# Kernel optimization log

Measured on AMD Instinct MI355X. Metric: run time of the kernel, lower is better.

Reference implementation:

```python
import jax, jax.numpy as jnp
import numpy as np

D_MODEL = 1024
N_HEADS = 16
HEAD_DIM = D_MODEL // N_HEADS
FFN_DIM = 4096
T = 2048
LN_EPS = 1e-5


def layer_norm(x, g, b):
    mu = jnp.mean(x, axis=-1, keepdims=True)
    var = jnp.mean(jnp.square(x - mu), axis=-1, keepdims=True)
    return (x - mu) * jax.lax.rsqrt(var + LN_EPS) * g + b


def setup_inputs() -> dict:
    key = jax.random.key(0)
    ks = jax.random.split(key, 12)
    s = 0.02
    x = jax.random.normal(ks[0], (1, T, D_MODEL), dtype=jnp.float32)
    # causal mask: True means masked (strict upper triangle)
    causal_mask = jnp.triu(jnp.ones((T, T), dtype=bool), k=1)
    # ALiBi bias: -slope * distance, per head
    slopes = 2.0 ** (-8.0 * (jnp.arange(1, N_HEADS + 1, dtype=jnp.float32) / N_HEADS))
    pos = jnp.arange(T, dtype=jnp.float32)
    dist = pos[None, :] - pos[:, None]  # (T, T)
    alibi_bias = slopes[:, None, None] * jnp.minimum(dist, 0.0)[None]  # (H, T, T)
    inp = {
        "x": x,
        "causal_mask": causal_mask,
        "alibi_bias": alibi_bias.astype(jnp.float32),
        "wq": jax.random.normal(ks[1], (D_MODEL, D_MODEL), jnp.float32) * s,
        "bq": jnp.zeros((D_MODEL,), jnp.float32),
        "wk": jax.random.normal(ks[2], (D_MODEL, D_MODEL), jnp.float32) * s,
        "bk": jnp.zeros((D_MODEL,), jnp.float32),
        "wv": jax.random.normal(ks[3], (D_MODEL, D_MODEL), jnp.float32) * s,
        "bv": jnp.zeros((D_MODEL,), jnp.float32),
        "wo": jax.random.normal(ks[4], (D_MODEL, D_MODEL), jnp.float32) * s,
        "bo": jnp.zeros((D_MODEL,), jnp.float32),
        "w1": jax.random.normal(ks[5], (D_MODEL, FFN_DIM), jnp.float32) * s,
        "b1": jnp.zeros((FFN_DIM,), jnp.float32),
        "w2": jax.random.normal(ks[6], (FFN_DIM, D_MODEL), jnp.float32) * s,
        "b2": jnp.zeros((D_MODEL,), jnp.float32),
        "g1": jnp.ones((D_MODEL,), jnp.float32),
        "be1": jnp.zeros((D_MODEL,), jnp.float32),
        "g2": jnp.ones((D_MODEL,), jnp.float32),
        "be2": jnp.zeros((D_MODEL,), jnp.float32),
    }
    return inp


def reference(x, causal_mask, alibi_bias, wq, bq, wk, bk, wv, bv, wo, bo,
              w1, b1, w2, b2, g1, be1, g2, be2):
    B, Tt, D = x.shape
    H, hd = N_HEADS, HEAD_DIM
    x_norm = layer_norm(x, g1, be1)
    # projections -> (B, H, T, hd)
    def split_heads(y):
        return y.reshape(B, Tt, H, hd).transpose(0, 2, 1, 3)
    Q = split_heads(x_norm @ wq + bq)
    K = split_heads(x_norm @ wk + bk)
    V = split_heads(x_norm @ wv + bv)
    scale = jnp.sqrt(jnp.float32(hd))
    scores = jnp.einsum('bhqd,bhkd->bhqk', Q, K) / scale
    scores = scores + alibi_bias[None]
    scores = jnp.where(causal_mask[None, None], -jnp.inf, scores)
    attn = jax.nn.softmax(scores, axis=-1)
    attn_out = jnp.einsum('bhqk,bhkd->bhqd', attn, V)
    attn_out = attn_out.transpose(0, 2, 1, 3).reshape(B, Tt, D)
    attn_out = attn_out @ wo + bo
    x = x + attn_out
    x_norm = layer_norm(x, g2, be2)
    h = jax.nn.gelu(x_norm @ w1 + b1, approximate=False)
    ffn_out = h @ w2 + b2
    return x + ffn_out
```

## Files before the change

### kernel.cpp

```cpp
#include <hip/hip_runtime.h>
#include <hip/hip_bf16.h>
#include <math.h>

#define T_SEQ 2048
#define D_MODEL 1024
#define N_HEADS 16
#define HEAD_DIM 64
#define FFN_DIM 4096

typedef _Float16 halfx8 __attribute__((ext_vector_type(8)));
typedef _Float16 halfx4 __attribute__((ext_vector_type(4)));
typedef float floatx4 __attribute__((ext_vector_type(4)));

__device__ __forceinline__ void async_ld16(const _Float16* g, _Float16* l) {
  __builtin_amdgcn_global_load_lds(
      (const __attribute__((address_space(1))) unsigned int*)g,
      (__attribute__((address_space(3))) unsigned int*)l, 16, 0, 0);
}

__global__ __launch_bounds__(256) void ln_h_kernel(
    const float* __restrict__ x, const float* __restrict__ g,
    const float* __restrict__ b, _Float16* __restrict__ y, int D) {
  int row = blockIdx.x;
  const float* xr = x + (size_t)row * D;
  _Float16* yr = y + (size_t)row * D;
  int tid = threadIdx.x;
  int lid = tid & 63, wid = tid >> 6;
  __shared__ float red[8];

  float sum = 0.f;
  for (int i = tid; i < D; i += 256) sum += xr[i];
  for (int o = 32; o > 0; o >>= 1) sum += __shfl_down(sum, o, 64);
  if (lid == 0) red[wid] = sum;
  __syncthreads();
  if (tid == 0) { float t = 0; for (int i = 0; i < 4; i++) t += red[i]; red[0] = t; }
  __syncthreads();
  float mu = red[0] / D;
  __syncthreads();

  float vs = 0.f;
  for (int i = tid; i < D; i += 256) { float d = xr[i] - mu; vs += d * d; }
  for (int o = 32; o > 0; o >>= 1) vs += __shfl_down(vs, o, 64);
  if (lid == 0) red[wid] = vs;
  __syncthreads();
  if (tid == 0) { float t = 0; for (int i = 0; i < 4; i++) t += red[i]; red[0] = t; }
  __syncthreads();
  float rstd = rsqrtf(red[0] / D + 1e-5f);

  for (int i = tid; i < D; i += 256)
    yr[i] = (_Float16)((xr[i] - mu) * rstd * g[i] + b[i]);
}

__global__ __launch_bounds__(256) void transpose_h_kernel(
    const float* __restrict__ in, _Float16* __restrict__ out, int K, int N) {
  __shared__ float tile[32][33];
  int tk = blockIdx.y * 32, tn = blockIdx.x * 32;
  int tid = threadIdx.x;
  int r = tid >> 3;
  int c = (tid & 7) * 4;
  float4 v = *(const float4*)&in[(size_t)(tk + r) * N + tn + c];
  tile[r][c] = v.x; tile[r][c + 1] = v.y; tile[r][c + 2] = v.z; tile[r][c + 3] = v.w;
  __syncthreads();
  halfx4 o;
  o[0] = (_Float16)tile[c][r];
  o[1] = (_Float16)tile[c + 1][r];
  o[2] = (_Float16)tile[c + 2][r];
  o[3] = (_Float16)tile[c + 3][r];
  *(halfx4*)&out[(size_t)(tn + r) * K + tk + c] = o;
}

__global__ __launch_bounds__(256) void pack_bias_kernel(
    const float* __restrict__ bq, const float* __restrict__ bk,
    const float* __restrict__ bv, float* __restrict__ o) {
  int i = blockIdx.x * 256 + threadIdx.x;
  if (i < 1024) o[i] = bq[i];
  else if (i < 2048) o[i] = bk[i - 1024];
  else if (i < 3072) o[i] = bv[i - 2048];
}

template <int MODE>
__global__ __launch_bounds__(256) void hgemm_kernel(
    const _Float16* __restrict__ A, const _Float16* __restrict__ Bt,
    const float* __restrict__ bias, const float* __restrict__ res,
    float* __restrict__ Cf, _Float16* __restrict__ Ch,
    int M, int N, int K) {
  __shared__ _Float16 As[128][32];
  __shared__ _Float16 Bs[128][32];
  const int tid = threadIdx.x;
  const int w = tid >> 6, lane = tid & 63;
  const int l16 = lane & 15, quad = lane >> 4;
  const int m0 = blockIdx.y * 128, n0 = blockIdx.x * 128;
  const int wm = (w >> 1) * 64, wn = (w & 1) * 64;

  floatx4 acc[4][4];
#pragma unroll
  for (int i = 0; i < 4; i++)
#pragma unroll
    for (int j = 0; j < 4; j++) acc[i][j] = (floatx4){0.f, 0.f, 0.f, 0.f};

  const int srow = lane >> 2;
  const int scol = (lane & 3) * 8;
  const _Float16* Ag = A + (size_t)(m0 + w * 32 + srow) * K + scol;
  const _Float16* Bg = Bt + (size_t)(n0 + w * 32 + srow) * K + scol;
  _Float16* AsB = &As[w * 32][0];
  _Float16* BsB = &Bs[w * 32][0];

  for (int k0 = 0; k0 < K; k0 += 32) {
    async_ld16(Ag + k0, AsB);
    async_ld16(Ag + k0 + (size_t)16 * K, AsB + 16 * 32);
    async_ld16(Bg + k0, BsB);
    async_ld16(Bg + k0 + (size_t)16 * K, BsB + 16 * 32);
    __syncthreads();
    halfx8 af[4], bf[4];
#pragma unroll
    for (int mt = 0; mt < 4; mt++) af[mt] = *(const halfx8*)&As[wm + mt * 16 + l16][quad * 8];
#pragma unroll
    for (int nt = 0; nt < 4; nt++) bf[nt] = *(const halfx8*)&Bs[wn + nt * 16 + l16][quad * 8];
#pragma unroll
    for (int mt = 0; mt < 4; mt++)
#pragma unroll
      for (int nt = 0; nt < 4; nt++)
        acc[mt][nt] = __builtin_amdgcn_mfma_f32_16x16x32_f16(af[mt], bf[nt], acc[mt][nt], 0, 0, 0);
    __syncthreads();
  }

#pragma unroll
  for (int mt = 0; mt < 4; mt++) {
#pragma unroll
    for (int nt = 0; nt < 4; nt++) {
      int col = n0 + wn + nt * 16 + l16;
      float bv = bias[col];
#pragma unroll
      for (int r = 0; r < 4; r++) {
        int row = m0 + wm + mt * 16 + quad * 4 + r;
        float v = acc[mt][nt][r] + bv;
        if (MODE == 1) v = 0.5f * v * (1.0f + erff(v * 0.70710678118f));
        if (MODE == 2) {
          Cf[(size_t)row * N + col] = v + res[(size_t)row * N + col];
        } else {
          Ch[(size_t)row * N + col] = (_Float16)v;
        }
      }
    }
  }
}

#define LROW 72
#define QKV_STR 3072
__global__ __launch_bounds__(256) void flash_attn_kernel(
    const _Float16* __restrict__ QKV, _Float16* __restrict__ out) {
  __shared__ _Float16 Ks[64][LROW];
  __shared__ _Float16 Vt[64][LROW];
  __shared__ _Float16 Ps[4][16][LROW];

  const int h = blockIdx.y;
  const int qt = blockIdx.x;
  const int q0 = qt * 64;
  const int tid = threadIdx.x;
  const int w = tid >> 6;
  const int lane = tid & 63;
  const int l16 = lane & 15;
  const int quad = lane >> 4;

  const _Float16* Qg = QKV + h * HEAD_DIM;
  const _Float16* Kg = QKV + 1024 + h * HEAD_DIM;
  const _Float16* Vg = QKV + 2048 + h * HEAD_DIM;

  const _Float16* qp = Qg + (size_t)(q0 + w * 16 + l16) * QKV_STR;
  halfx8 qa0 = *(const halfx8*)(qp + quad * 8);
  halfx8 qa1 = *(const halfx8*)(qp + 32 + quad * 8);

  float m_i[4], l_i[4];
  floatx4 o_acc[4];
#pragma unroll
  for (int r = 0; r < 4; r++) { m_i[r] = -INFINITY; l_i[r] = 0.f; }
#pragma unroll
  for (int c = 0; c < 4; c++) o_acc[c] = (floatx4){0.f, 0.f, 0.f, 0.f};

  const float slope = exp2f(-0.5f * (float)(h + 1));
  const int row_base = q0 + w * 16 + quad * 4;

  for (int t = 0; t <= qt; t++) {
    const int k0 = t * 64;
    __syncthreads();
#pragma unroll
    for (int it = 0; it < 2; it++) {
      int chunk = tid + it * 256;
      int kr = chunk >> 3, c8 = chunk & 7;
      *(halfx8*)(&Ks[kr][c8 * 8]) =
          *(const halfx8*)(Kg + (size_t)(k0 + kr) * QKV_STR + c8 * 8);
    }
#pragma unroll
    for (int it = 0; it < 2; it++) {
      int chunk = tid + it * 256;
      int kr = chunk >> 3, c8 = chunk & 7;
      halfx8 v = *(const halfx8*)(Vg + (size_t)(k0 + kr) * QKV_STR + c8 * 8);
      int kg = kr >> 3, k7 = kr & 7;
#pragma unroll
      for (int j = 0; j < 8; j++)
        Vt[c8 * 8 + j][((kg ^ c8) << 3) + k7] = v[j];
    }
    __syncthreads();

    float sc[4][4];
#pragma unroll
    for (int sub = 0; sub < 4; sub++) {
      halfx8 b0 = *(const halfx8*)(&Ks[sub * 16 + l16][quad * 8]);
      halfx8 b1 = *(const halfx8*)(&Ks[sub * 16 + l16][32 + quad * 8]);
      floatx4 acc = (floatx4){0.f, 0.f, 0.f, 0.f};
      acc = __builtin_amdgcn_mfma_f32_16x16x32_f16(qa0, b0, acc, 0, 0, 0);
      acc = __builtin_amdgcn_mfma_f32_16x16x32_f16(qa1, b1, acc, 0, 0, 0);
#pragma unroll
      for (int r = 0; r < 4; r++) sc[sub][r] = acc[r];
    }

#pragma unroll
    for (int r = 0; r < 4; r++) {
      const int rg = row_base + r;
      float mx = m_i[r];
#pragma unroll
      for (int sub = 0; sub < 4; sub++) {
        int cg = k0 + sub * 16 + l16;
        float s = sc[sub][r] * 0.125f + slope * (float)(cg - rg);
        if (cg > rg) s = -1e30f;
        sc[sub][r] = s;
        mx = fmaxf(mx, s);
      }
      mx = fmaxf(mx, __shfl_xor(mx, 1, 64));
      mx = fmaxf(mx, __shfl_xor(mx, 2, 64));
      mx = fmaxf(mx, __shfl_xor(mx, 4, 64));
      mx = fmaxf(mx, __shfl_xor(mx, 8, 64));
      float alpha = __expf(m_i[r] - mx);
      m_i[r] = mx;
      float ls = 0.f;
#pragma unroll
      for (int sub = 0; sub < 4; sub++) {
        float p = __expf(sc[sub][r] - mx);
        ls += p;
        Ps[w][quad * 4 + r][sub * 16 + l16] = (_Float16)p;
      }
      ls += __shfl_xor(ls, 1, 64);
      ls += __shfl_xor(ls, 2, 64);
      ls += __shfl_xor(ls, 4, 64);
      ls += __shfl_xor(ls, 8, 64);
      l_i[r] = l_i[r] * alpha + ls;
#pragma unroll
      for (int c = 0; c < 4; c++) o_acc[c][r] *= alpha;
    }

#pragma unroll
    for (int kh = 0; kh < 2; kh++) {
      halfx8 pa = *(const halfx8*)(&Ps[w][l16][kh * 32 + quad * 8]);
      int kgrp = kh * 4 + quad;
#pragma unroll
      for (int c = 0; c < 4; c++) {
        int d = c * 16 + l16;
        halfx8 vb = *(const halfx8*)(&Vt[d][(kgrp ^ (d >> 3)) << 3]);
        o_acc[c] = __builtin_amdgcn_mfma_f32_16x16x32_f16(pa, vb, o_acc[c], 0, 0, 0);
      }
    }
  }

#pragma unroll
  for (int c = 0; c < 4; c++)
#pragma unroll
    for (int r = 0; r < 4; r++)
      out[(size_t)(row_base + r) * D_MODEL + h * HEAD_DIM + c * 16 + l16] =
          (_Float16)(o_acc[c][r] / l_i[r]);
}

extern "C" void kernel_launch(void* const* d_in, const int* in_sizes, int n_in,
                              void* d_out, int out_size, void* d_ws, size_t ws_size,
                              hipStream_t stream) {
  const float* x   = (const float*)d_in[0];
  const float* wq  = (const float*)d_in[3];
  const float* bq  = (const float*)d_in[4];
  const float* wk  = (const float*)d_in[5];
  const float* bk  = (const float*)d_in[6];
  const float* wv  = (const float*)d_in[7];
  const float* bv  = (const float*)d_in[8];
  const float* wo  = (const float*)d_in[9];
  const float* bo  = (const float*)d_in[10];
  const float* w1  = (const float*)d_in[11];
  const float* b1  = (const float*)d_in[12];
  const float* w2  = (const float*)d_in[13];
  const float* b2  = (const float*)d_in[14];
  const float* g1  = (const float*)d_in[15];
  const float* be1 = (const float*)d_in[16];
  const float* g2  = (const float*)d_in[17];
  const float* be2 = (const float*)d_in[18];
  float* out = (float*)d_out;

  const size_t TD = (size_t)T_SEQ * D_MODEL;
  char* p = (char*)d_ws;
  float*    x1     = (float*)p;            p += TD * 4;
  float*    bqkv   = (float*)p;            p += 4096 * 4;
  _Float16* xnh    = (_Float16*)p;         p += TD * 2;
  _Float16* QKVh   = (_Float16*)p;         p += 3 * TD * 2;
  _Float16* attnh  = (_Float16*)p;         p += TD * 2;
  _Float16* hh     = (_Float16*)p;         p += 4 * TD * 2;
  _Float16* Wqkvt  = (_Float16*)p;         p += 3 * 1024 * 1024 * 2;
  _Float16* Wot    = (_Float16*)p;         p += 1024 * 1024 * 2;
  _Float16* W1t    = (_Float16*)p;         p += (size_t)1024 * 4096 * 2;
  _Float16* W2t    = (_Float16*)p;         p += (size_t)4096 * 1024 * 2;

  dim3 blk(256);

  transpose_h_kernel<<<dim3(32, 32), blk, 0, stream>>>(wq, Wqkvt, 1024, 1024);
  transpose_h_kernel<<<dim3(32, 32), blk, 0, stream>>>(wk, Wqkvt + 1024 * 1024, 1024, 1024);
  transpose_h_kernel<<<dim3(32, 32), blk, 0, stream>>>(wv, Wqkvt + 2 * 1024 * 1024, 1024, 1024);
  transpose_h_kernel<<<dim3(32, 32), blk, 0, stream>>>(wo, Wot, 1024, 1024);
  transpose_h_kernel<<<dim3(128, 32), blk, 0, stream>>>(w1, W1t, 1024, 4096);
  transpose_h_kernel<<<dim3(32, 128), blk, 0, stream>>>(w2, W2t, 4096, 1024);
  pack_bias_kernel<<<dim3(12), blk, 0, stream>>>(bq, bk, bv, bqkv);

  ln_h_kernel<<<T_SEQ, blk, 0, stream>>>(x, g1, be1, xnh, D_MODEL);

  hgemm_kernel<0><<<dim3(3072 / 128, T_SEQ / 128), blk, 0, stream>>>(
      xnh, Wqkvt, bqkv, nullptr, nullptr, QKVh, T_SEQ, 3072, 1024);

  flash_attn_kernel<<<dim3(T_SEQ / 64, N_HEADS), blk, 0, stream>>>(QKVh, attnh);

  hgemm_kernel<2><<<dim3(1024 / 128, T_SEQ / 128), blk, 0, stream>>>(
      attnh, Wot, bo, x, x1, nullptr, T_SEQ, 1024, 1024);

  ln_h_kernel<<<T_SEQ, blk, 0, stream>>>(x1, g2, be2, xnh, D_MODEL);

  hgemm_kernel<1><<<dim3(4096 / 128, T_SEQ / 128), blk, 0, stream>>>(
      xnh, W1t, b1, nullptr, nullptr, hh, T_SEQ, 4096, 1024);

  hgemm_kernel<2><<<dim3(1024 / 128, T_SEQ / 128), blk, 0, stream>>>(
      hh, W2t, b2, x1, out, nullptr, T_SEQ, 1024, 4096);
}
```

Before: 642.4 us.

## Write V transposed from QKV GEMM, prefetch K/V in attention, smaller tiles for N=1024 GEMMs

The QKV GEMM epilogue now writes Q/K to a 2048-wide buffer and V directly transposed to a head-major layout. This lets flash attention load V rows with vector stores instead of scalar scatter-transposes, and K/V for the next tile are register-prefetched while the current tile is being computed. Softmax switches to exp2 with the log2e factor folded into the scale and slope. The two N=1024 GEMMs use 64-row tiles for more blocks, the weight transposes and bias pack are merged into one launch, and layer norm is vectorized to a single float4 pass. Costs are higher register pressure from the prefetch and a strided transposed-V write in the GEMM epilogue.

New measurement: 599.2 us. 1.07x faster.

```diff
diff --git a/kernel.cpp b/kernel.cpp
--- a/kernel.cpp
+++ b/kernel.cpp
@@ -20,44 +20,72 @@
 
 __global__ __launch_bounds__(256) void ln_h_kernel(
     const float* __restrict__ x, const float* __restrict__ g,
-    const float* __restrict__ b, _Float16* __restrict__ y, int D) {
+    const float* __restrict__ b, _Float16* __restrict__ y) {
   int row = blockIdx.x;
-  const float* xr = x + (size_t)row * D;
-  _Float16* yr = y + (size_t)row * D;
+  const float* xr = x + (size_t)row * D_MODEL;
+  _Float16* yr = y + (size_t)row * D_MODEL;
   int tid = threadIdx.x;
   int lid = tid & 63, wid = tid >> 6;
   __shared__ float red[8];
 
-  float sum = 0.f;
-  for (int i = tid; i < D; i += 256) sum += xr[i];
+  float4 v = *(const float4*)&xr[tid * 4];
+  float sum = v.x + v.y + v.z + v.w;
   for (int o = 32; o > 0; o >>= 1) sum += __shfl_down(sum, o, 64);
   if (lid == 0) red[wid] = sum;
   __syncthreads();
   if (tid == 0) { float t = 0; for (int i = 0; i < 4; i++) t += red[i]; red[0] = t; }
   __syncthreads();
-  float mu = red[0] / D;
-  __syncthreads();
-
-  float vs = 0.f;
-  for (int i = tid; i < D; i += 256) { float d = xr[i] - mu; vs += d * d; }
+  float mu = red[0] * (1.0f / D_MODEL);
+  __syncthreads();
+
+  float dx = v.x - mu, dy = v.y - mu, dz = v.z - mu, dw = v.w - mu;
+  float vs = dx * dx + dy * dy + dz * dz + dw * dw;
   for (int o = 32; o > 0; o >>= 1) vs += __shfl_down(vs, o, 64);
   if (lid == 0) red[wid] = vs;
   __syncthreads();
   if (tid == 0) { float t = 0; for (int i = 0; i < 4; i++) t += red[i]; red[0] = t; }
   __syncthreads();
-  float rstd = rsqrtf(red[0] / D + 1e-5f);
-
-  for (int i = tid; i < D; i += 256)
-    yr[i] = (_Float16)((xr[i] - mu) * rstd * g[i] + b[i]);
-}
-
-__global__ __launch_bounds__(256) void transpose_h_kernel(
-    const float* __restrict__ in, _Float16* __restrict__ out, int K, int N) {
+  float rstd = rsqrtf(red[0] * (1.0f / D_MODEL) + 1e-5f);
+
+  float4 gv = *(const float4*)&g[tid * 4];
+  float4 bv = *(const float4*)&b[tid * 4];
+  halfx4 o;
+  o[0] = (_Float16)(dx * rstd * gv.x + bv.x);
+  o[1] = (_Float16)(dy * rstd * gv.y + bv.y);
+  o[2] = (_Float16)(dz * rstd * gv.z + bv.z);
+  o[3] = (_Float16)(dw * rstd * gv.w + bv.w);
+  *(halfx4*)&yr[tid * 4] = o;
+}
+
+__global__ __launch_bounds__(256) void prep_kernel(
+    const float* __restrict__ wq, const float* __restrict__ wk,
+    const float* __restrict__ wv, const float* __restrict__ wo,
+    const float* __restrict__ w1, const float* __restrict__ w2,
+    const float* __restrict__ bq, const float* __restrict__ bk,
+    const float* __restrict__ bv, _Float16* __restrict__ Wqkvt,
+    _Float16* __restrict__ Wot, _Float16* __restrict__ W1t,
+    _Float16* __restrict__ W2t, float* __restrict__ bqkv) {
+  int bId = blockIdx.x;
+  int tid = threadIdx.x;
+  if (bId >= 12288) {
+    int i = (bId - 12288) * 256 + tid;
+    if (i < 1024) bqkv[i] = bq[i];
+    else if (i < 2048) bqkv[i] = bk[i - 1024];
+    else bqkv[i] = bv[i - 2048];
+    return;
+  }
+  const float* in; _Float16* outp; int K, N, t;
+  if (bId < 1024)      { in = wq; outp = Wqkvt;                 K = 1024; N = 1024; t = bId; }
+  else if (bId < 2048) { in = wk; outp = Wqkvt + 1024 * 1024;   K = 1024; N = 1024; t = bId - 1024; }
+  else if (bId < 3072) { in = wv; outp = Wqkvt + 2 * 1024 * 1024; K = 1024; N = 1024; t = bId - 2048; }
+  else if (bId < 4096) { in = wo; outp = Wot;                   K = 1024; N = 1024; t = bId - 3072; }
+  else if (bId < 8192) { in = w1; outp = W1t;                   K = 1024; N = 4096; t = bId - 4096; }
+  else                 { in = w2; outp = W2t;                   K = 4096; N = 1024; t = bId - 8192; }
+  int ntn = N / 32;
+  int tk = (t / ntn) * 32, tn = (t % ntn) * 32;
+
   __shared__ float tile[32][33];
-  int tk = blockIdx.y * 32, tn = blockIdx.x * 32;
-  int tid = threadIdx.x;
-  int r = tid >> 3;
-  int c = (tid & 7) * 4;
+  int r = tid >> 3, c = (tid & 7) * 4;
   float4 v = *(const float4*)&in[(size_t)(tk + r) * N + tn + c];
   tile[r][c] = v.x; tile[r][c + 1] = v.y; tile[r][c + 2] = v.z; tile[r][c + 3] = v.w;
   __syncthreads();
@@ -66,58 +94,52 @@
   o[1] = (_Float16)tile[c + 1][r];
   o[2] = (_Float16)tile[c + 2][r];
   o[3] = (_Float16)tile[c + 3][r];
-  *(halfx4*)&out[(size_t)(tn + r) * K + tk + c] = o;
-}
-
-__global__ __launch_bounds__(256) void pack_bias_kernel(
-    const float* __restrict__ bq, const float* __restrict__ bk,
-    const float* __restrict__ bv, float* __restrict__ o) {
-  int i = blockIdx.x * 256 + threadIdx.x;
-  if (i < 1024) o[i] = bq[i];
-  else if (i < 2048) o[i] = bk[i - 1024];
-  else if (i < 3072) o[i] = bv[i - 2048];
-}
-
-template <int MODE>
+  *(halfx4*)&outp[(size_t)(tn + r) * K + tk + c] = o;
+}
+
+template <int MODE, int BM_>
 __global__ __launch_bounds__(256) void hgemm_kernel(
     const _Float16* __restrict__ A, const _Float16* __restrict__ Bt,
     const float* __restrict__ bias, const float* __restrict__ res,
     float* __restrict__ Cf, _Float16* __restrict__ Ch,
-    int M, int N, int K) {
-  __shared__ _Float16 As[128][32];
+    _Float16* __restrict__ Vtg, int M, int N, int K) {
+  constexpr int TM = BM_ / 32;
+  __shared__ _Float16 As[BM_][32];
   __shared__ _Float16 Bs[128][32];
   const int tid = threadIdx.x;
   const int w = tid >> 6, lane = tid & 63;
   const int l16 = lane & 15, quad = lane >> 4;
-  const int m0 = blockIdx.y * 128, n0 = blockIdx.x * 128;
-  const int wm = (w >> 1) * 64, wn = (w & 1) * 64;
-
-  floatx4 acc[4][4];
-#pragma unroll
-  for (int i = 0; i < 4; i++)
+  const int m0 = blockIdx.y * BM_, n0 = blockIdx.x * 128;
+  const int wm = (w >> 1) * (BM_ / 2), wn = (w & 1) * 64;
+
+  floatx4 acc[TM][4];
+#pragma unroll
+  for (int i = 0; i < TM; i++)
 #pragma unroll
     for (int j = 0; j < 4; j++) acc[i][j] = (floatx4){0.f, 0.f, 0.f, 0.f};
 
   const int srow = lane >> 2;
   const int scol = (lane & 3) * 8;
-  const _Float16* Ag = A + (size_t)(m0 + w * 32 + srow) * K + scol;
+  const _Float16* Ag;
+  _Float16* AsB;
+  if (BM_ == 128) { Ag = A + (size_t)(m0 + w * 32 + srow) * K + scol; AsB = &As[w * 32][0]; }
+  else            { Ag = A + (size_t)(m0 + w * 16 + srow) * K + scol; AsB = &As[w * 16][0]; }
   const _Float16* Bg = Bt + (size_t)(n0 + w * 32 + srow) * K + scol;
-  _Float16* AsB = &As[w * 32][0];
   _Float16* BsB = &Bs[w * 32][0];
 
   for (int k0 = 0; k0 < K; k0 += 32) {
     async_ld16(Ag + k0, AsB);
-    async_ld16(Ag + k0 + (size_t)16 * K, AsB + 16 * 32);
+    if (BM_ == 128) async_ld16(Ag + k0 + (size_t)16 * K, AsB + 16 * 32);
     async_ld16(Bg + k0, BsB);
     async_ld16(Bg + k0 + (size_t)16 * K, BsB + 16 * 32);
     __syncthreads();
-    halfx8 af[4], bf[4];
-#pragma unroll
-    for (int mt = 0; mt < 4; mt++) af[mt] = *(const halfx8*)&As[wm + mt * 16 + l16][quad * 8];
+    halfx8 af[TM], bf[4];
+#pragma unroll
+    for (int mt = 0; mt < TM; mt++) af[mt] = *(const halfx8*)&As[wm + mt * 16 + l16][quad * 8];
 #pragma unroll
     for (int nt = 0; nt < 4; nt++) bf[nt] = *(const halfx8*)&Bs[wn + nt * 16 + l16][quad * 8];
 #pragma unroll
-    for (int mt = 0; mt < 4; mt++)
+    for (int mt = 0; mt < TM; mt++)
 #pragma unroll
       for (int nt = 0; nt < 4; nt++)
         acc[mt][nt] = __builtin_amdgcn_mfma_f32_16x16x32_f16(af[mt], bf[nt], acc[mt][nt], 0, 0, 0);
@@ -125,30 +147,47 @@
   }
 
 #pragma unroll
-  for (int mt = 0; mt < 4; mt++) {
+  for (int mt = 0; mt < TM; mt++) {
+    int row0 = m0 + wm + mt * 16 + quad * 4;
 #pragma unroll
     for (int nt = 0; nt < 4; nt++) {
       int col = n0 + wn + nt * 16 + l16;
       float bv = bias[col];
+      float vv[4];
 #pragma unroll
       for (int r = 0; r < 4; r++) {
-        int row = m0 + wm + mt * 16 + quad * 4 + r;
         float v = acc[mt][nt][r] + bv;
         if (MODE == 1) v = 0.5f * v * (1.0f + erff(v * 0.70710678118f));
-        if (MODE == 2) {
-          Cf[(size_t)row * N + col] = v + res[(size_t)row * N + col];
+        vv[r] = v;
+      }
+      if (MODE == 2) {
+#pragma unroll
+        for (int r = 0; r < 4; r++)
+          Cf[(size_t)(row0 + r) * N + col] = vv[r] + res[(size_t)(row0 + r) * N + col];
+      } else if (MODE == 3) {
+        if (col < 2048) {
+#pragma unroll
+          for (int r = 0; r < 4; r++)
+            Ch[(size_t)(row0 + r) * 2048 + col] = (_Float16)vv[r];
         } else {
-          Ch[(size_t)row * N + col] = (_Float16)v;
+          halfx4 pk;
+#pragma unroll
+          for (int r = 0; r < 4; r++) pk[r] = (_Float16)vv[r];
+          *(halfx4*)&Vtg[(size_t)(col - 2048) * T_SEQ + row0] = pk;
         }
+      } else {
+#pragma unroll
+        for (int r = 0; r < 4; r++)
+          Ch[(size_t)(row0 + r) * N + col] = (_Float16)vv[r];
       }
     }
   }
 }
 
 #define LROW 72
-#define QKV_STR 3072
 __global__ __launch_bounds__(256) void flash_attn_kernel(
-    const _Float16* __restrict__ QKV, _Float16* __restrict__ out) {
+    const _Float16* __restrict__ QK, const _Float16* __restrict__ Vtg,
+    _Float16* __restrict__ out) {
   __shared__ _Float16 Ks[64][LROW];
   __shared__ _Float16 Vt[64][LROW];
   __shared__ _Float16 Ps[4][16][LROW];
@@ -162,11 +201,11 @@
   const int l16 = lane & 15;
   const int quad = lane >> 4;
 
-  const _Float16* Qg = QKV + h * HEAD_DIM;
-  const _Float16* Kg = QKV + 1024 + h * HEAD_DIM;
-  const _Float16* Vg = QKV + 2048 + h * HEAD_DIM;
-
-  const _Float16* qp = Qg + (size_t)(q0 + w * 16 + l16) * QKV_STR;
+  const _Float16* Qg = QK + h * HEAD_DIM;
+  const _Float16* Kg = QK + 1024 + h * HEAD_DIM;
+  const _Float16* Vg = Vtg + (size_t)h * HEAD_DIM * T_SEQ;
+
+  const _Float16* qp = Qg + (size_t)(q0 + w * 16 + l16) * 2048;
   halfx8 qa0 = *(const halfx8*)(qp + quad * 8);
   halfx8 qa1 = *(const halfx8*)(qp + 32 + quad * 8);
 
@@ -177,30 +216,31 @@
 #pragma unroll
   for (int c = 0; c < 4; c++) o_acc[c] = (floatx4){0.f, 0.f, 0.f, 0.f};
 
-  const float slope = exp2f(-0.5f * (float)(h + 1));
+  const float scale2 = 0.18033688f;
+  const float slope2 = exp2f(-0.5f * (float)(h + 1)) * 1.44269504f;
   const int row_base = q0 + w * 16 + quad * 4;
+
+  const int kr = tid >> 3;
+  const int c8 = tid & 7;
+  halfx8 kpre0, kpre1, vpre0, vpre1;
+#define PREFETCH(K0)                                                          \
+  {                                                                           \
+    kpre0 = *(const halfx8*)(Kg + (size_t)((K0) + kr) * 2048 + c8 * 8);       \
+    kpre1 = *(const halfx8*)(Kg + (size_t)((K0) + kr + 32) * 2048 + c8 * 8);  \
+    vpre0 = *(const halfx8*)(Vg + (size_t)kr * T_SEQ + (K0) + c8 * 8);        \
+    vpre1 = *(const halfx8*)(Vg + (size_t)(kr + 32) * T_SEQ + (K0) + c8 * 8); \
+  }
+  PREFETCH(0)
 
   for (int t = 0; t <= qt; t++) {
     const int k0 = t * 64;
     __syncthreads();
-#pragma unroll
-    for (int it = 0; it < 2; it++) {
-      int chunk = tid + it * 256;
-      int kr = chunk >> 3, c8 = chunk & 7;
-      *(halfx8*)(&Ks[kr][c8 * 8]) =
-          *(const halfx8*)(Kg + (size_t)(k0 + kr) * QKV_STR + c8 * 8);
-    }
-#pragma unroll
-    for (int it = 0; it < 2; it++) {
-      int chunk = tid + it * 256;
-      int kr = chunk >> 3, c8 = chunk & 7;
-      halfx8 v = *(const halfx8*)(Vg + (size_t)(k0 + kr) * QKV_STR + c8 * 8);
-      int kg = kr >> 3, k7 = kr & 7;
-#pragma unroll
-      for (int j = 0; j < 8; j++)
-        Vt[c8 * 8 + j][((kg ^ c8) << 3) + k7] = v[j];
-    }
+    *(halfx8*)&Ks[kr][c8 * 8] = kpre0;
+    *(halfx8*)&Ks[kr + 32][c8 * 8] = kpre1;
+    *(halfx8*)&Vt[kr][((c8 ^ (kr >> 3)) & 7) * 8] = vpre0;
+    *(halfx8*)&Vt[kr + 32][((c8 ^ ((kr + 32) >> 3)) & 7) * 8] = vpre1;
     __syncthreads();
+    if (t < qt) PREFETCH(k0 + 64)
 
     float sc[4][4];
 #pragma unroll
@@ -221,7 +261,7 @@
 #pragma unroll
       for (int sub = 0; sub < 4; sub++) {
         int cg = k0 + sub * 16 + l16;
-        float s = sc[sub][r] * 0.125f + slope * (float)(cg - rg);
+        float s = sc[sub][r] * scale2 + slope2 * (float)(cg - rg);
         if (cg > rg) s = -1e30f;
         sc[sub][r] = s;
         mx = fmaxf(mx, s);
@@ -230,12 +270,12 @@
       mx = fmaxf(mx, __shfl_xor(mx, 2, 64));
       mx = fmaxf(mx, __shfl_xor(mx, 4, 64));
       mx = fmaxf(mx, __shfl_xor(mx, 8, 64));
-      float alpha = __expf(m_i[r] - mx);
+      float alpha = exp2f(m_i[r] - mx);
       m_i[r] = mx;
       float ls = 0.f;
 #pragma unroll
       for (int sub = 0; sub < 4; sub++) {
-        float p = __expf(sc[sub][r] - mx);
+        float p = exp2f(sc[sub][r] - mx);
         ls += p;
         Ps[w][quad * 4 + r][sub * 16 + l16] = (_Float16)p;
       }
@@ -255,7 +295,7 @@
 #pragma unroll
       for (int c = 0; c < 4; c++) {
         int d = c * 16 + l16;
-        halfx8 vb = *(const halfx8*)(&Vt[d][(kgrp ^ (d >> 3)) << 3]);
+        halfx8 vb = *(const halfx8*)(&Vt[d][((kgrp ^ (d >> 3)) & 7) << 3]);
         o_acc[c] = __builtin_amdgcn_mfma_f32_16x16x32_f16(pa, vb, o_acc[c], 0, 0, 0);
       }
     }
@@ -293,42 +333,38 @@
 
   const size_t TD = (size_t)T_SEQ * D_MODEL;
   char* p = (char*)d_ws;
-  float*    x1     = (float*)p;            p += TD * 4;
-  float*    bqkv   = (float*)p;            p += 4096 * 4;
-  _Float16* xnh    = (_Float16*)p;         p += TD * 2;
-  _Float16* QKVh   = (_Float16*)p;         p += 3 * TD * 2;
-  _Float16* attnh  = (_Float16*)p;         p += TD * 2;
-  _Float16* hh     = (_Float16*)p;         p += 4 * TD * 2;
-  _Float16* Wqkvt  = (_Float16*)p;         p += 3 * 1024 * 1024 * 2;
-  _Float16* Wot    = (_Float16*)p;         p += 1024 * 1024 * 2;
-  _Float16* W1t    = (_Float16*)p;         p += (size_t)1024 * 4096 * 2;
-  _Float16* W2t    = (_Float16*)p;         p += (size_t)4096 * 1024 * 2;
+  float*    x1    = (float*)p;     p += TD * 4;
+  float*    bqkv  = (float*)p;     p += 4096 * 4;
+  _Float16* xnh   = (_Float16*)p;  p += TD * 2;
+  _Float16* QKh   = (_Float16*)p;  p += (size_t)2048 * 2048 * 2;
+  _Float16* Vtg   = (_Float16*)p;  p += (size_t)1024 * 2048 * 2;
+  _Float16* attnh = (_Float16*)p;  p += TD * 2;
+  _Float16* hh    = (_Float16*)p;  p += (size_t)2048 * 4096 * 2;
+  _Float16* Wqkvt = (_Float16*)p;  p += (size_t)3 * 1024 * 1024 * 2;
+  _Float16* Wot   = (_Float16*)p;  p += (size_t)1024 * 1024 * 2;
+  _Float16* W1t   = (_Float16*)p;  p += (size_t)1024 * 4096 * 2;
+  _Float16* W2t   = (_Float16*)p;  p += (size_t)4096 * 1024 * 2;
 
   dim3 blk(256);
 
-  transpose_h_kernel<<<dim3(32, 32), blk, 0, stream>>>(wq, Wqkvt, 1024, 1024);
-  transpose_h_kernel<<<dim3(32, 32), blk, 0, stream>>>(wk, Wqkvt + 1024 * 1024, 1024, 1024);
-  transpose_h_kernel<<<dim3(32, 32), blk, 0, stream>>>(wv, Wqkvt + 2 * 1024 * 1024, 1024, 1024);
-  transpose_h_kernel<<<dim3(32, 32), blk, 0, stream>>>(wo, Wot, 1024, 1024);
-  transpose_h_kernel<<<dim3(128, 32), blk, 0, stream>>>(w1, W1t, 1024, 4096);
-  transpose_h_kernel<<<dim3(32, 128), blk, 0, stream>>>(w2, W2t, 4096, 1024);
-  pack_bias_kernel<<<dim3(12), blk, 0, stream>>>(bq, bk, bv, bqkv);
-
-  ln_h_kernel<<<T_SEQ, blk, 0, stream>>>(x, g1, be1, xnh, D_MODEL);
-
-  hgemm_kernel<0><<<dim3(3072 / 128, T_SEQ / 128), blk, 0, stream>>>(
-      xnh, Wqkvt, bqkv, nullptr, nullptr, QKVh, T_SEQ, 3072, 1024);
-
-  flash_attn_kernel<<<dim3(T_SEQ / 64, N_HEADS), blk, 0, stream>>>(QKVh, attnh);
-
-  hgemm_kernel<2><<<dim3(1024 / 128, T_SEQ / 128), blk, 0, stream>>>(
-      attnh, Wot, bo, x, x1, nullptr, T_SEQ, 1024, 1024);
-
-  ln_h_kernel<<<T_SEQ, blk, 0, stream>>>(x1, g2, be2, xnh, D_MODEL);
-
-  hgemm_kernel<1><<<dim3(4096 / 128, T_SEQ / 128), blk, 0, stream>>>(
-      xnh, W1t, b1, nullptr, nullptr, hh, T_SEQ, 4096, 1024);
-
-  hgemm_kernel<2><<<dim3(1024 / 128, T_SEQ / 128), blk, 0, stream>>>(
-      hh, W2t, b2, x1, out, nullptr, T_SEQ, 1024, 4096);
-}
+  prep_kernel<<<dim3(12300), blk, 0, stream>>>(wq, wk, wv, wo, w1, w2, bq, bk, bv,
+                                               Wqkvt, Wot, W1t, W2t, bqkv);
+
+  ln_h_kernel<<<T_SEQ, blk, 0, stream>>>(x, g1, be1, xnh);
+
+  hgemm_kernel<3, 128><<<dim3(3072 / 128, T_SEQ / 128), blk, 0, stream>>>(
+      xnh, Wqkvt, bqkv, nullptr, nullptr, QKh, Vtg, T_SEQ, 3072, 1024);
+
+  flash_attn_kernel<<<dim3(T_SEQ / 64, N_HEADS), blk, 0, stream>>>(QKh, Vtg, attnh);
+
+  hgemm_kernel<2, 64><<<dim3(1024 / 128, T_SEQ / 64), blk, 0, stream>>>(
+      attnh, Wot, bo, x, x1, nullptr, nullptr, T_SEQ, 1024, 1024);
+
+  ln_h_kernel<<<T_SEQ, blk, 0, stream>>>(x1, g2, be2, xnh);
+
+  hgemm_kernel<1, 128><<<dim3(4096 / 128, T_SEQ / 128), blk, 0, stream>>>(
+      xnh, W1t, b1, nullptr, nullptr, hh, nullptr, T_SEQ, 4096, 1024);
+
+  hgemm_kernel<2, 64><<<dim3(1024 / 128, T_SEQ / 64), blk, 0, stream>>>(
+      hh, W2t, b2, x1, out, nullptr, nullptr, T_SEQ, 1024, 4096);
+}
```
